# Kernel tuning notes

Measured on AMD Instinct MI355X. Metric: run time of the kernel, lower is better.

## Reference

```python
import jax, jax.numpy as jnp
import numpy as np

V, H, L, B, T = 128, 1024, 2, 64, 512

def setup_inputs() -> dict:
    key = jax.random.key(0)
    ks = jax.random.split(key, 6)
    idx = jax.random.randint(ks[0], (B, T), 0, V, dtype=jnp.int32)
    embed = jax.random.normal(ks[1], (V, H), dtype=jnp.float32) * 0.02
    Wx = jax.random.normal(ks[2], (L, H, 4 * H), dtype=jnp.float32) * (1.0 / np.sqrt(H))
    Wh = jax.random.normal(ks[3], (L, H, 4 * H), dtype=jnp.float32) * (1.0 / np.sqrt(H))
    b = jnp.zeros((L, 4 * H), dtype=jnp.float32)
    W_out = jax.random.normal(ks[4], (H, V), dtype=jnp.float32) * (1.0 / np.sqrt(H))
    return {"idx": idx, "embed": embed, "Wx": Wx, "Wh": Wh, "b": b, "W_out": W_out}

def reference(idx, embed, Wx, Wh, b, W_out):
    # idx: (B,T) int32; embed: (V,H); Wx,Wh: (L,H,4H); b: (L,4H); W_out: (H,V)
    x = embed[idx]                      # (B,T,H)
    Bv, Tv, Hv = x.shape
    Lv = Wx.shape[0]
    c0 = jnp.zeros((Lv, Bv, Hv), dtype=x.dtype)
    h0 = jnp.zeros((Lv, Bv, Hv), dtype=x.dtype)

    def step(carry, x_t):
        c, h = carry                    # each (L,B,H)
        new_c, new_h = [], []
        h_in = x_t                      # (B,H)
        for i in range(Lv):             # fixed small layer count
            gates = h_in @ Wx[i] + h[i] @ Wh[i] + b[i]   # (B,4H)
            i_g, f_g, g_g, o_g = jnp.split(gates, 4, axis=-1)
            c_new = jax.nn.sigmoid(f_g) * c[i] + jax.nn.sigmoid(i_g) * jnp.tanh(g_g)
            h_new = jax.nn.sigmoid(o_g) * jnp.tanh(c_new)
            new_c.append(c_new)
            new_h.append(h_new)
            h_in = h_new                # eval mode: dropout mask == 1
        return (jnp.stack(new_c), jnp.stack(new_h)), h_in

    _, hs_tm = jax.lax.scan(step, (c0, h0), jnp.swapaxes(x, 0, 1))  # (T,B,H)
    hs = jnp.swapaxes(hs_tm, 0, 1)                                  # (B,T,H)
    return hs @ W_out                                               # (B,T,V)
```

## Files before the change

kernel.cpp:

```cpp
#include <hip/hip_runtime.h>
#include <math.h>

#define Hn 1024
#define Gn 4096
#define Bn 64
#define Tn 512
#define Vn 128
#define NWG 196
#define NPH 515
#define HSLOTB 131072
#define NGRP 7
#define GRPSZ 28

typedef float f32x16 __attribute__((ext_vector_type(16)));
typedef int i32x16 __attribute__((ext_vector_type(16)));
typedef int i32x4 __attribute__((ext_vector_type(4)));
typedef long i64x2 __attribute__((ext_vector_type(2)));
typedef unsigned long long u64;

#define MFMAI8(a, b, c) __builtin_amdgcn_mfma_i32_32x32x16_i8(a, b, c, 0, 0, 0)

#define QSCALE 32256.0f
#define C1K (65536.0f / (QSCALE * QSCALE))
#define C23K (256.0f / (QSCALE * QSCALE))

__device__ __forceinline__ float coh_loadf(const float* p) {
  return __hip_atomic_load(p, __ATOMIC_RELAXED, __HIP_MEMORY_SCOPE_AGENT);
}
__device__ __forceinline__ void coh_storef(float* p, float v) {
  __hip_atomic_store(p, v, __ATOMIC_RELAXED, __HIP_MEMORY_SCOPE_AGENT);
}
__device__ __forceinline__ void coh_storeu(unsigned* p, unsigned v) {
  __hip_atomic_store(p, v, __ATOMIC_RELAXED, __HIP_MEMORY_SCOPE_AGENT);
}

#define A_LOAD16(dst, ptr) \
  asm volatile("global_load_dwordx4 %0, %1, off sc1" : "=v"(dst) : "v"(ptr))

__device__ __forceinline__ float sigf(float x) {
  float e = exp2f(x * -1.442695040888963f);
  return __fdividef(1.f, 1.f + e);
}
__device__ __forceinline__ float tanh_(float x) {
  x = fminf(fmaxf(x, -15.f), 15.f);
  float e = exp2f(x * -2.885390081777926f);
  return __fdividef(1.f - e, 1.f + e);
}
__device__ __forceinline__ int clampq(int v) {
  return v > 32255 ? 32255 : (v < -32255 ? -32255 : v);
}

__global__ void ew0_kernel(const float* __restrict__ embed, const float* __restrict__ Wx0,
                           const float* __restrict__ bias, float* __restrict__ EW0) {
  int n = blockIdx.x * 256 + threadIdx.x;
  int vb = blockIdx.y * 8;
  float acc[8] = {0, 0, 0, 0, 0, 0, 0, 0};
  for (int k = 0; k < Hn; k++) {
    float w = Wx0[(size_t)k * Gn + n];
#pragma unroll
    for (int i = 0; i < 8; i++)
      acc[i] = fmaf(embed[(vb + i) * Hn + k], w, acc[i]);
  }
  float bb = bias[n];
#pragma unroll
  for (int i = 0; i < 8; i++)
    EW0[(size_t)(vb + i) * Gn + n] = acc[i] + bb;
}

__device__ __forceinline__ void gridbar(unsigned* bar, int p, int b) {
  asm volatile("s_waitcnt vmcnt(0)" ::: "memory");
  __syncthreads();
  if (threadIdx.x == 0) {
    unsigned* gcnt = bar + (b / GRPSZ) * 32;
    unsigned* ccnt = bar + 256;
    unsigned* flag = bar + 288;
    const unsigned tgt = (unsigned)(p + 1);
    unsigned old = __hip_atomic_fetch_add(gcnt, 1u, __ATOMIC_RELAXED, __HIP_MEMORY_SCOPE_AGENT);
    bool released = false;
    if (old == (unsigned)GRPSZ * tgt - 1u) {
      unsigned c = __hip_atomic_fetch_add(ccnt, 1u, __ATOMIC_RELAXED, __HIP_MEMORY_SCOPE_AGENT);
      if (c == (unsigned)NGRP * tgt - 1u) {
        __hip_atomic_store(flag, tgt, __ATOMIC_RELAXED, __HIP_MEMORY_SCOPE_AGENT);
        released = true;
      }
    }
    if (!released) {
      while (__hip_atomic_load(flag, __ATOMIC_RELAXED, __HIP_MEMORY_SCOPE_AGENT) < tgt)
        __builtin_amdgcn_s_sleep(2);
    }
  }
  __syncthreads();
}

__global__ __launch_bounds__(512, 1)
void persist_kernel(const int* __restrict__ idx,
                    const float* __restrict__ Wx, const float* __restrict__ Wh,
                    const float* __restrict__ bias, const float* __restrict__ Wout,
                    const float* __restrict__ EW0,
                    unsigned char* __restrict__ h0f, unsigned char* __restrict__ h1f,
                    float* __restrict__ P, float* __restrict__ out,
                    unsigned* __restrict__ bar) {
  extern __shared__ char smem[];
  unsigned char* bqhi = (unsigned char*)smem;
  unsigned char* bqlo = (unsigned char*)(smem + 65536);
  float* xg = (float*)(smem + 131072);
  float* cb = (float*)(smem + 131072 + 17408);

  const int b = blockIdx.x, tid = threadIdx.x;
  const int wv = tid >> 6, l = tid & 63;
  const int type = (b < 64) ? 0 : (b < 128) ? 1 : (b < 192) ? 2 : 3;
  const int i = b - ((type == 0) ? 0 : (type == 1) ? 64 : (type == 2) ? 128 : 192);
  const int mtv = wv & 1, khv = wv >> 1;
  const int c32 = l & 31, o8 = (l >> 5) * 8;

  const float* Wsrc = (type == 0) ? Wh
                    : (type == 1) ? (Wx + (size_t)Hn * Gn)
                    : (type == 2) ? (Wh + (size_t)Hn * Gn) : Wout;

  {
    float pmax0 = 0.f, pmax1 = 0.f;
    if (type < 3) {
      for (int nt = 0; nt < 2; nt++) {
        int colv = (c32 >> 3) * Hn + 16 * i + nt * 8 + (c32 & 7);
        float pm = 0.f;
        for (int kk = 0; kk < 8; kk++) {
          int ks = wv * 8 + kk;
#pragma unroll
          for (int e = 0; e < 8; e++)
            pm = fmaxf(pm, fabsf(Wsrc[(size_t)(ks * 16 + o8 + e) * Gn + colv]));
        }
        if (nt) pmax1 = pm; else pmax0 = pm;
      }
    } else {
      int colv = 32 * i + c32;
      for (int kk = 0; kk < 8; kk++) {
        int ks = wv * 8 + kk;
#pragma unroll
        for (int e = 0; e < 8; e++)
          pmax0 = fmaxf(pmax0, fabsf(Wout[(size_t)(ks * 16 + o8 + e) * Vn + colv]));
      }
      pmax1 = 1.f;
    }
    int g = wv * 2 + (l >> 5);
    xg[g * 64 + c32] = pmax0;
    xg[g * 64 + 32 + c32] = pmax1;
  }
  __syncthreads();
  if (tid < 64) {
    float s = 1e-20f;
    for (int g = 0; g < 16; g++) s = fmaxf(s, xg[g * 64 + tid]);
    xg[1024 + tid] = s;
  }
  __syncthreads();
  const float sc0 = xg[1024 + c32], sc1 = xg[1024 + 32 + c32];
  const float qs0 = QSCALE / sc0, qs1 = QSCALE / sc1;
  const float c1v0 = sc0 * C1K, c1v1 = sc1 * C1K;
  const float c23v0 = sc0 * C23K, c23v1 = sc1 * C23K;
  __syncthreads();

  {
    const int ntN = (type < 3) ? 2 : 1;
    for (int nt = 0; nt < ntN; nt++) {
      int colv; size_t stride;
      if (type < 3) { colv = (c32 >> 3) * Hn + 16 * i + nt * 8 + (c32 & 7); stride = Gn; }
      else { colv = 32 * i + c32; stride = Vn; }
      float qs = nt ? qs1 : qs0;
      for (int kk = 0; kk < 8; kk++) {
        int ks = wv * 8 + kk;
        u64 hq = 0, lq = 0;
#pragma unroll
        for (int e = 0; e < 8; e++) {
          float w = Wsrc[(size_t)(ks * 16 + o8 + e) * stride + colv];
          int Wi = clampq((int)rintf(w * qs));
          int bh = (Wi + 128) >> 8;
          int bl = Wi - (bh << 8);
          hq |= (u64)(unsigned char)(bh & 0xFF) << (8 * e);
          lq |= (u64)(unsigned char)(bl & 0xFF) << (8 * e);
        }
        size_t off = ((size_t)nt * 64 + ks) * 512 + (size_t)l * 8;
        *(u64*)(bqhi + off) = hq;
        *(u64*)(bqlo + off) = lq;
      }
    }
  }
  for (int q = tid; q < 1024; q += 512) cb[q] = 0.f;

  const int ujl0 = (tid >> 6) << 2;
  const int ur = tid & 63;
  const int untc = ujl0 >> 3;
  float bb4[16];
  if (type == 2 && tid < 256) {
#pragma unroll
    for (int q = 0; q < 4; ++q) {
      int j = 16 * i + ujl0 + q;
#pragma unroll
      for (int g = 0; g < 4; ++g) bb4[q * 4 + g] = bias[Gn + g * Hn + j];
    }
  }
  __syncthreads();

  for (int p = 0; p < NPH; ++p) {
    const int sA = (p + 1) & 1;
    int t; bool active;
    if (type == 0)      { t = p;     active = (t < Tn); }
    else if (type == 1) { t = p - 1; active = (t >= 0 && t < Tn); }
    else if (type == 2) { t = p - 2; active = (t >= 0 && t < Tn); }
    else                { t = p - 3; active = (t >= 0 && t < Tn); }

    if (active) {
      float pre[16];
      if (type == 0 && tid < 256) {
        const int v = idx[ur * Tn + t];
        const float* er = EW0 + (size_t)v * Gn + 16 * i + ujl0;
#pragma unroll
        for (int q = 0; q < 4; ++q)
#pragma unroll
          for (int g = 0; g < 4; ++g)
            pre[q * 4 + g] = coh_loadf(er + q + g * Hn);
      } else if (type == 2 && tid < 256) {
        const float* pr = P + ((size_t)(t & 1) * 64 + i) * 4096 + ur * 64 + untc * 32;
#pragma unroll
        for (int q = 0; q < 4; ++q)
#pragma unroll
          for (int g = 0; g < 4; ++g)
            pre[q * 4 + g] = coh_loadf(pr + g * 8 + ((ujl0 & 7) + q));
      }

      const unsigned char* A = ((type <= 1) ? h0f : h1f) + (size_t)sA * HSLOTB;
      const unsigned char* ab = A + (size_t)mtv * 1024 + (size_t)l * 16;
      const int ks0 = khv * 16;
      i32x4 av[16];
#pragma unroll
      for (int k2 = 0; k2 < 16; ++k2) {
        const unsigned char* ap = ab + (size_t)(ks0 + k2) * 2048;
        A_LOAD16(av[k2], ap);
      }
      asm volatile("s_waitcnt vmcnt(0)" ::: "memory");
      __builtin_amdgcn_sched_barrier(0);

      i32x16 p1a = {}, p23a = {}, p1b = {}, p23b = {};
#pragma unroll
      for (int k2 = 0; k2 < 16; ++k2) {
        const int ks = ks0 + k2;
        i64x2 aq = __builtin_bit_cast(i64x2, av[k2]);
        long ahi = aq[0], alo = aq[1];
        size_t bo = (size_t)ks * 512 + (size_t)l * 8;
        long bh0 = *(const long*)(bqhi + bo);
        long bl0 = *(const long*)(bqlo + bo);
        p1a = MFMAI8(ahi, bh0, p1a);
        p23a = MFMAI8(ahi, bl0, p23a);
        p23a = MFMAI8(alo, bh0, p23a);
        if (type < 3) {
          long bh1 = *(const long*)(bqhi + bo + 32768);
          long bl1 = *(const long*)(bqlo + bo + 32768);
          p1b = MFMAI8(ahi, bh1, p1b);
          p23b = MFMAI8(ahi, bl1, p23b);
          p23b = MFMAI8(alo, bh1, p23b);
        }
      }
      f32x16 acc0, acc1;
#pragma unroll
      for (int r = 0; r < 16; ++r) {
        acc0[r] = c1v0 * (float)p1a[r] + c23v0 * (float)p23a[r];
        acc1[r] = (type < 3) ? (c1v1 * (float)p1b[r] + c23v1 * (float)p23b[r]) : 0.f;
      }

#pragma unroll
      for (int rd = 1; rd < 4; ++rd) {
        if (khv == rd) {
          float* s0 = xg + (mtv * 2 + 0) * 1024 + l;
          float* s1 = xg + (mtv * 2 + 1) * 1024 + l;
#pragma unroll
          for (int r = 0; r < 16; ++r) { s0[r * 64] = acc0[r]; s1[r * 64] = acc1[r]; }
        }
        __syncthreads();
        if (khv == 0) {
          const float* s0 = xg + (mtv * 2 + 0) * 1024 + l;
          const float* s1 = xg + (mtv * 2 + 1) * 1024 + l;
#pragma unroll
          for (int r = 0; r < 16; ++r) { acc0[r] += s0[r * 64]; acc1[r] += s1[r * 64]; }
        }
        __syncthreads();
      }

      if (type == 1) {
        if (khv == 0) {
          float* pp = P + ((size_t)(t & 1) * 64 + i) * 4096;
#pragma unroll
          for (int r = 0; r < 16; ++r) {
            int row = (r & 3) + 8 * (r >> 2) + 4 * (l >> 5) + 32 * mtv;
            coh_storef(pp + row * 64 + (l & 31), acc0[r]);
            coh_storef(pp + row * 64 + 32 + (l & 31), acc1[r]);
          }
        }
      } else if (type == 3) {
        if (khv == 0) {
#pragma unroll
          for (int r = 0; r < 16; ++r) {
            int row = (r & 3) + 8 * (r >> 2) + 4 * (l >> 5) + 32 * mtv;
            coh_storef(out + ((size_t)row * Tn + t) * Vn + 32 * i + (l & 31), acc0[r]);
          }
        }
      } else {
        if (khv == 0) {
#pragma unroll
          for (int r = 0; r < 16; ++r) {
            int row = (r & 3) + 8 * (r >> 2) + 4 * (l >> 5) + 32 * mtv;
            xg[row * 65 + (l & 31)] = acc0[r];
            xg[row * 65 + 32 + (l & 31)] = acc1[r];
          }
        }
        __syncthreads();
        unsigned char* dst = ((type == 0) ? h0f : h1f) + (size_t)(p & 1) * HSLOTB;
        if (tid < 256) {
          unsigned hiw = 0, low = 0;
#pragma unroll
          for (int q = 0; q < 4; ++q) {
            int jl = ujl0 + q;
            int jo = jl & 7;
            float gi_ = xg[ur * 65 + untc * 32 + jo];
            float gf_ = xg[ur * 65 + untc * 32 + 8 + jo];
            float gg_ = xg[ur * 65 + untc * 32 + 16 + jo];
            float go_ = xg[ur * 65 + untc * 32 + 24 + jo];
            if (type == 0) {
              gi_ += pre[q * 4 + 0];
              gf_ += pre[q * 4 + 1];
              gg_ += pre[q * 4 + 2];
              go_ += pre[q * 4 + 3];
            } else {
              gi_ += pre[q * 4 + 0] + bb4[q * 4 + 0];
              gf_ += pre[q * 4 + 1] + bb4[q * 4 + 1];
              gg_ += pre[q * 4 + 2] + bb4[q * 4 + 2];
              go_ += pre[q * 4 + 3] + bb4[q * 4 + 3];
            }
            float c_ = cb[jl * 64 + ur];
            float cn = sigf(gf_) * c_ + sigf(gi_) * tanh_(gg_);
            float hn = sigf(go_) * tanh_(cn);
            cb[jl * 64 + ur] = cn;
            int Hq = clampq((int)rintf(hn * QSCALE));
            int ah8 = (Hq + 128) >> 8;
            int al8 = Hq - (ah8 << 8);
            hiw |= ((unsigned)(unsigned char)(ah8 & 0xFF)) << (8 * q);
            low |= ((unsigned)(unsigned char)(al8 & 0xFF)) << (8 * q);
          }
          const int lt = (ur & 31) | ((ujl0 >> 3) << 5);
          const int e0 = ujl0 & 7;
          const int mtt = ur >> 5;
          size_t offh = ((size_t)i * 2 + mtt) * 1024 + (size_t)lt * 16 + e0;
          coh_storeu((unsigned*)(dst + offh), hiw);
          coh_storeu((unsigned*)(dst + offh + 8), low);
        }
      }
    }
    gridbar(bar, p, b);
  }
}

extern "C" void kernel_launch(void* const* d_in, const int* in_sizes, int n_in,
                              void* d_out, int out_size, void* d_ws, size_t ws_size,
                              hipStream_t stream) {
  const int* idx = (const int*)d_in[0];
  const float* embed = (const float*)d_in[1];
  const float* Wx = (const float*)d_in[2];
  const float* Wh = (const float*)d_in[3];
  const float* bias = (const float*)d_in[4];
  const float* Wout = (const float*)d_in[5];
  float* out = (float*)d_out;

  float* EW0 = (float*)d_ws;
  unsigned char* h0f = (unsigned char*)(EW0 + 524288);
  unsigned char* h1f = h0f + 2 * HSLOTB;
  float* P = (float*)(h1f + 2 * HSLOTB);
  unsigned* bar = (unsigned*)(P + 524288);

  hipMemsetAsync(h0f, 0, (size_t)4 * HSLOTB, stream);
  hipMemsetAsync(bar, 0, 4096, stream);

  ew0_kernel<<<dim3(Gn / 256, Vn / 8), 256, 0, stream>>>(embed, Wx, bias, EW0);

  hipFuncSetAttribute((const void*)persist_kernel,
                      hipFuncAttributeMaxDynamicSharedMemorySize, 152576);

  void* args[] = {(void*)&idx, (void*)&Wx, (void*)&Wh, (void*)&bias, (void*)&Wout,
                  (void*)&EW0, (void*)&h0f, (void*)&h1f,
                  (void*)&P, (void*)&out, (void*)&bar};
  hipLaunchCooperativeKernel((const void*)persist_kernel, dim3(NWG), dim3(512),
                             args, 152576, stream);

  (void)embed; (void)in_sizes; (void)n_in; (void)out_size; (void)ws_size;
}
```

Before: 7.462 ms.

## Replicate hidden-state buffers per XCD and read A operands from local copies

Each phase, the blocks on each XCD cooperatively copy the current h0/h1 quantized state slots into a per-XCD replica buffer. A per-XCD arrival counter then synchronizes those blocks before anyone proceeds. The MFMA A-operand loads read from the replica with sc0 instead of sc1, so repeated reads can hit the XCD-local L2 instead of going through coherent memory. In exchange it adds an extra copy pass and an extra intra-XCD barrier every phase, plus a startup grid barrier to count blocks per XCD.

```diff
diff --git a/kernel.cpp b/kernel.cpp
--- a/kernel.cpp
+++ b/kernel.cpp
@@ -11,6 +11,8 @@
 #define HSLOTB 131072
 #define NGRP 7
 #define GRPSZ 28
+#define XCNT_OFF 320
+#define XARR_OFF 576
 
 typedef float f32x16 __attribute__((ext_vector_type(16)));
 typedef int i32x16 __attribute__((ext_vector_type(16)));
@@ -33,9 +35,18 @@
 __device__ __forceinline__ void coh_storeu(unsigned* p, unsigned v) {
   __hip_atomic_store(p, v, __ATOMIC_RELAXED, __HIP_MEMORY_SCOPE_AGENT);
 }
+__device__ __forceinline__ u64 coh_loadq(const u64* p) {
+  return __hip_atomic_load(p, __ATOMIC_RELAXED, __HIP_MEMORY_SCOPE_AGENT);
+}
 
 #define A_LOAD16(dst, ptr) \
-  asm volatile("global_load_dwordx4 %0, %1, off sc1" : "=v"(dst) : "v"(ptr))
+  asm volatile("global_load_dwordx4 %0, %1, off sc0" : "=v"(dst) : "v"(ptr))
+
+__device__ __forceinline__ int xcc_id() {
+  int x;
+  asm("s_getreg_b32 %0, hwreg(HW_REG_XCC_ID)" : "=s"(x));
+  return x & 7;
+}
 
 __device__ __forceinline__ float sigf(float x) {
   float e = exp2f(x * -1.442695040888963f);
@@ -67,14 +78,13 @@
     EW0[(size_t)(vb + i) * Gn + n] = acc[i] + bb;
 }
 
-__device__ __forceinline__ void gridbar(unsigned* bar, int p, int b) {
+__device__ __forceinline__ void gridbar(unsigned* bar, unsigned tgt, int b) {
   asm volatile("s_waitcnt vmcnt(0)" ::: "memory");
   __syncthreads();
   if (threadIdx.x == 0) {
     unsigned* gcnt = bar + (b / GRPSZ) * 32;
     unsigned* ccnt = bar + 256;
     unsigned* flag = bar + 288;
-    const unsigned tgt = (unsigned)(p + 1);
     unsigned old = __hip_atomic_fetch_add(gcnt, 1u, __ATOMIC_RELAXED, __HIP_MEMORY_SCOPE_AGENT);
     bool released = false;
     if (old == (unsigned)GRPSZ * tgt - 1u) {
@@ -98,6 +108,7 @@
                     const float* __restrict__ bias, const float* __restrict__ Wout,
                     const float* __restrict__ EW0,
                     unsigned char* __restrict__ h0f, unsigned char* __restrict__ h1f,
+                    unsigned char* __restrict__ replPool,
                     float* __restrict__ P, float* __restrict__ out,
                     unsigned* __restrict__ bar) {
   extern __shared__ char smem[];
@@ -105,6 +116,7 @@
   unsigned char* bqlo = (unsigned char*)(smem + 65536);
   float* xg = (float*)(smem + 131072);
   float* cb = (float*)(smem + 131072 + 17408);
+  __shared__ int sh_xcd, sh_rank, sh_cnt;
 
   const int b = blockIdx.x, tid = threadIdx.x;
   const int wv = tid >> 6, l = tid & 63;
@@ -199,8 +211,50 @@
   }
   __syncthreads();
 
+  if (tid == 0) {
+    int x = xcc_id();
+    sh_xcd = x;
+    sh_rank = (int)__hip_atomic_fetch_add(bar + XCNT_OFF + x * 32, 1u,
+                                          __ATOMIC_RELAXED, __HIP_MEMORY_SCOPE_AGENT);
+  }
+  __syncthreads();
+  gridbar(bar, 1u, b);
+  if (tid == 0)
+    sh_cnt = (int)__hip_atomic_load(bar + XCNT_OFF + sh_xcd * 32,
+                                    __ATOMIC_RELAXED, __HIP_MEMORY_SCOPE_AGENT);
+  __syncthreads();
+  const int myxcd = sh_xcd, myrank = sh_rank, xcnt = sh_cnt;
+  unsigned char* repl = replPool + (size_t)myxcd * 2 * HSLOTB;
+
   for (int p = 0; p < NPH; ++p) {
     const int sA = (p + 1) & 1;
+
+    {
+      const unsigned char* s0 = h0f + (size_t)sA * HSLOTB;
+      const unsigned char* s1 = h1f + (size_t)sA * HSLOTB;
+      for (int tI = myrank; tI < 32; tI += xcnt) {
+        const unsigned char* src = (tI < 16) ? s0 + (size_t)tI * 8192
+                                             : s1 + (size_t)(tI - 16) * 8192;
+        unsigned char* dstp = repl + ((tI < 16) ? (size_t)tI * 8192
+                                                : (size_t)HSLOTB + (size_t)(tI - 16) * 8192);
+        const u64* sp = (const u64*)(src + (size_t)tid * 16);
+        u64 qa = coh_loadq(sp);
+        u64 qb = coh_loadq(sp + 1);
+        u64* dp = (u64*)(dstp + (size_t)tid * 16);
+        dp[0] = qa; dp[1] = qb;
+      }
+    }
+    asm volatile("s_waitcnt vmcnt(0)" ::: "memory");
+    __syncthreads();
+    if (tid == 0) {
+      unsigned* xa = bar + XARR_OFF + myxcd * 32;
+      __hip_atomic_fetch_add(xa, 1u, __ATOMIC_RELAXED, __HIP_MEMORY_SCOPE_AGENT);
+      const unsigned tgt2 = (unsigned)xcnt * (unsigned)(p + 1);
+      while (__hip_atomic_load(xa, __ATOMIC_RELAXED, __HIP_MEMORY_SCOPE_AGENT) < tgt2)
+        __builtin_amdgcn_s_sleep(1);
+    }
+    __syncthreads();
+
     int t; bool active;
     if (type == 0)      { t = p;     active = (t < Tn); }
     else if (type == 1) { t = p - 1; active = (t >= 0 && t < Tn); }
@@ -208,6 +262,18 @@
     else                { t = p - 3; active = (t >= 0 && t < Tn); }
 
     if (active) {
+      const unsigned char* A = repl + ((type <= 1) ? 0 : (size_t)HSLOTB);
+      const unsigned char* ab = A + (size_t)mtv * 1024 + (size_t)l * 16;
+      const int ks0 = khv * 16;
+      i32x4 av[16];
+#pragma unroll
+      for (int k2 = 0; k2 < 16; ++k2) {
+        const unsigned char* ap = ab + (size_t)(ks0 + k2) * 2048;
+        A_LOAD16(av[k2], ap);
+      }
+      asm volatile("s_waitcnt vmcnt(0)" ::: "memory");
+      __builtin_amdgcn_sched_barrier(0);
+
       float pre[16];
       if (type == 0 && tid < 256) {
         const int v = idx[ur * Tn + t];
@@ -225,18 +291,6 @@
           for (int g = 0; g < 4; ++g)
             pre[q * 4 + g] = coh_loadf(pr + g * 8 + ((ujl0 & 7) + q));
       }
-
-      const unsigned char* A = ((type <= 1) ? h0f : h1f) + (size_t)sA * HSLOTB;
-      const unsigned char* ab = A + (size_t)mtv * 1024 + (size_t)l * 16;
-      const int ks0 = khv * 16;
-      i32x4 av[16];
-#pragma unroll
-      for (int k2 = 0; k2 < 16; ++k2) {
-        const unsigned char* ap = ab + (size_t)(ks0 + k2) * 2048;
-        A_LOAD16(av[k2], ap);
-      }
-      asm volatile("s_waitcnt vmcnt(0)" ::: "memory");
-      __builtin_amdgcn_sched_barrier(0);
 
       i32x16 p1a = {}, p23a = {}, p1b = {}, p23b = {};
 #pragma unroll
@@ -352,7 +406,7 @@
         }
       }
     }
-    gridbar(bar, p, b);
+    gridbar(bar, (unsigned)(p + 2), b);
   }
 }
 
@@ -371,7 +425,8 @@
   unsigned char* h0f = (unsigned char*)(EW0 + 524288);
   unsigned char* h1f = h0f + 2 * HSLOTB;
   float* P = (float*)(h1f + 2 * HSLOTB);
-  unsigned* bar = (unsigned*)(P + 524288);
+  unsigned char* replPool = (unsigned char*)(P + 524288);
+  unsigned* bar = (unsigned*)(replPool + (size_t)8 * 2 * HSLOTB);
 
   hipMemsetAsync(h0f, 0, (size_t)4 * HSLOTB, stream);
   hipMemsetAsync(bar, 0, 4096, stream);
@@ -382,7 +437,7 @@
                       hipFuncAttributeMaxDynamicSharedMemorySize, 152576);
 
   void* args[] = {(void*)&idx, (void*)&Wx, (void*)&Wh, (void*)&bias, (void*)&Wout,
-                  (void*)&EW0, (void*)&h0f, (void*)&h1f,
+                  (void*)&EW0, (void*)&h0f, (void*)&h1f, (void*)&replPool,
                   (void*)&P, (void*)&out, (void*)&bar};
   hipLaunchCooperativeKernel((const void*)persist_kernel, dim3(NWG), dim3(512),
                              args, 152576, stream);
```

Measured after the change: 13.07 ms. 1.75x slower.
